# Performance work log

Measured on AMD Instinct MI355X. Metric: run time of the kernel, lower is better.

The kernel has to match this reference:

```python
import jax, jax.numpy as jnp
import numpy as np

G = 2   # FlipGroup order
H = 16  # num_heads
TEMPERATURE = 1.0


def _shared_w(A, B):
    # Z2 regular-representation equivariant linear: block-circulant weight
    # W = [[A, B], [B, A]], shape (dim, dim)
    return jnp.concatenate([
        jnp.concatenate([A, B], axis=1),
        jnp.concatenate([B, A], axis=1),
    ], axis=0)


def setup_inputs() -> dict:
    key = jax.random.key(0)
    ks = jax.random.split(key, 9)
    d = 1024
    dh = d // G
    inp = {"x": jax.random.normal(ks[0], (4, 1024, d), jnp.float32)}
    for i, n in enumerate(["wqA", "wqB", "wkA", "wkB", "wvA", "wvB", "wpA", "wpB"]):
        inp[n] = jax.random.normal(ks[i + 1], (dh, dh), jnp.float32) * 0.02
    return inp


def reference(x, wqA, wqB, wkA, wkB, wvA, wvB, wpA, wpB):
    B, N, C = x.shape
    hd = C // G // H            # per-group-channel head dim
    scale = hd ** -0.5

    q = x @ _shared_w(wqA, wqB).T
    k = x @ _shared_w(wkA, wkB).T
    v = x @ _shared_w(wvA, wvB).T

    def split(t):
        # (B,N,C) -> (B,H,G,N,hd): per-head features split into G group channels
        return t.reshape(B, N, H, G, hd).transpose(0, 2, 3, 1, 4)

    q, k, v = split(q), split(k), split(v)

    # per-channel attention: independent softmax per (head, group-channel)
    attn = jax.nn.softmax(
        jnp.einsum('bhgnd,bhgmd->bhgnm', q, k) * (scale / TEMPERATURE), axis=-1)
    o = jnp.einsum('bhgnm,bhgmd->bhgnd', attn, v)

    o = o.transpose(0, 3, 1, 2, 4).reshape(B, N, C)
    return o @ _shared_w(wpA, wpB).T
```

## Files before the change

kernel.cpp:

```cpp
#include <hip/hip_runtime.h>


typedef unsigned short ushort_t;
typedef __attribute__((ext_vector_type(4))) unsigned short ushort4_t;
typedef __attribute__((ext_vector_type(8))) unsigned short ushort8;
typedef __attribute__((ext_vector_type(8))) __bf16 bf16x8;
typedef __attribute__((ext_vector_type(4))) float f32x4;
typedef __attribute__((ext_vector_type(4))) unsigned int uint4_t;

#define GPTR(p) ((const __attribute__((address_space(1))) void*)(p))
#define LPTR(p) ((__attribute__((address_space(3))) void*)(p))

static __device__ __forceinline__ unsigned short f2b(float f) {
  unsigned int u = __builtin_bit_cast(unsigned int, f);
  unsigned int r = u + 0x7fffu + ((u >> 16) & 1u);
  return (unsigned short)(r >> 16);
}
static __device__ __forceinline__ float b2f(ushort_t h) {
  unsigned int u = ((unsigned int)h) << 16;
  return __builtin_bit_cast(float, u);
}
static __device__ __forceinline__ unsigned int pack2_rtna(float a, float b) {
  const unsigned int ra = __builtin_bit_cast(unsigned int, a) + 0x8000u;
  const unsigned int rb = __builtin_bit_cast(unsigned int, b) + 0x8000u;
  return __builtin_amdgcn_perm(rb, ra, 0x07060302u);
}

__global__ __launch_bounds__(256) void prep_k(
    const float* __restrict__ x,
    const float* __restrict__ wqA, const float* __restrict__ wqB,
    const float* __restrict__ wkA, const float* __restrict__ wkB,
    const float* __restrict__ wvA, const float* __restrict__ wvB,
    const float* __restrict__ wpA, const float* __restrict__ wpB,
    ushort_t* __restrict__ xsd, ushort_t* __restrict__ Wsd, float sclq) {
  const int bid = blockIdx.x;
  if (bid < 1024) {
    const int u = bid * 256 + threadIdx.x;
    const int m = u >> 6;
    const int k8 = (u & 63) * 8;
    const float* p1 = x + (size_t)m * 1024 + k8;
    const float* p2 = p1 + 512;
    const f32x4 a0 = *(const f32x4*)p1,  a1 = *(const f32x4*)(p1 + 4);
    const f32x4 b0 = *(const f32x4*)p2,  b1 = *(const f32x4*)(p2 + 4);
    ushort8 vs, vd;
#pragma unroll
    for (int e = 0; e < 4; ++e) {
      vs[e] = f2b(a0[e] + b0[e]); vs[e + 4] = f2b(a1[e] + b1[e]);
      vd[e] = f2b(a0[e] - b0[e]); vd[e + 4] = f2b(a1[e] - b1[e]);
    }
    *(ushort8*)&xsd[(size_t)m * 1024 + k8] = vs;
    *(ushort8*)&xsd[(size_t)m * 1024 + 512 + k8] = vd;
  } else {
    const int u = (bid - 1024) * 256 + threadIdx.x;
    const int hm = u >> 15;
    const int rem = u & 32767;
    const int r = rem >> 6;
    const int c8 = (rem & 63) * 8;
    const int proj = hm >> 1, isD = hm & 1;
    const float* A; const float* B;
    if (proj == 0)      { A = wqA; B = wqB; }
    else if (proj == 1) { A = wkA; B = wkB; }
    else if (proj == 2) { A = wvA; B = wvB; }
    else                { A = wpA; B = wpB; }
    const float scl = 0.5f * (proj == 0 ? sclq : 1.0f);
    const f32x4 a0 = *(const f32x4*)(A + (size_t)r * 512 + c8);
    const f32x4 a1 = *(const f32x4*)(A + (size_t)r * 512 + c8 + 4);
    const f32x4 b0 = *(const f32x4*)(B + (size_t)r * 512 + c8);
    const f32x4 b1 = *(const f32x4*)(B + (size_t)r * 512 + c8 + 4);
    ushort8 v;
#pragma unroll
    for (int e = 0; e < 4; ++e) {
      v[e]     = f2b(isD ? (a0[e] - b0[e]) * scl : (a0[e] + b0[e]) * scl);
      v[e + 4] = f2b(isD ? (a1[e] - b1[e]) * scl : (a1[e] + b1[e]) * scl);
    }
    *(ushort8*)&Wsd[(size_t)(proj * 1024 + isD * 512 + r) * 512 + c8] = v;
  }
}

__global__ __launch_bounds__(256, 3) void gemm_sd_qkv(const ushort_t* __restrict__ xsd,
                                                      const ushort_t* __restrict__ Wsd,
                                                      ushort_t* __restrict__ Qb,
                                                      ushort_t* __restrict__ Kb,
                                                      ushort_t* __restrict__ Vtb) {
  __shared__ ushort_t sh[24576];

  const int t = threadIdx.x;
  const int wid = t >> 6, lane = t & 63;
  const int wm = wid >> 1, half = wid & 1;
  const int lr = lane & 15, lg = lane >> 4;

  const int bid = blockIdx.x;
  const int c = bid & 7, j = bid >> 3;
  const int mt = c * 4 + (j & 3);
  const int nzt = j >> 2;
  const int z = nzt >> 3;
  const int n0 = (nzt & 7) * 64;
  const int m0 = mt * 128;

  f32x4 acc[4][4];
  const f32x4 fz = {0.f, 0.f, 0.f, 0.f};
#pragma unroll
  for (int mf = 0; mf < 4; ++mf)
#pragma unroll
    for (int nf = 0; nf < 4; ++nf) acc[mf][nf] = fz;

#define ISSUE(kt_, s_)                                                                   \
  {                                                                                      \
    ushort_t* base_ = sh + (s_) * 12288;                                                 \
    const int k0_ = (kt_) * 32;                                                          \
    _Pragma("unroll") for (int rnd = 0; rnd < 2; ++rnd) {                                \
      const int ch = rnd * 256 + t;                                                      \
      const int row = ch >> 2, cs = ch & 3;                                              \
      const int gcol = k0_ + ((cs ^ ((row >> 1) & 3)) << 3);                             \
      __builtin_amdgcn_global_load_lds(GPTR(xsd + (size_t)(m0 + row) * 1024 + gcol),     \
                                       LPTR(base_ + (size_t)ch * 8), 16, 0, 0);          \
      __builtin_amdgcn_global_load_lds(GPTR(xsd + (size_t)(m0 + row) * 1024 + 512 + gcol),\
                                       LPTR(base_ + 4096 + (size_t)ch * 8), 16, 0, 0);   \
    }                                                                                    \
    {                                                                                    \
      const int row = t >> 2, cs = t & 3;                                                \
      const int gcol = k0_ + ((cs ^ ((row >> 1) & 3)) << 3);                             \
      __builtin_amdgcn_global_load_lds(                                                  \
          GPTR(Wsd + (size_t)(z * 1024 + n0 + row) * 512 + gcol),                        \
          LPTR(sh + (s_) * 12288 + 8192 + (size_t)t * 8), 16, 0, 0);                     \
      __builtin_amdgcn_global_load_lds(                                                  \
          GPTR(Wsd + (size_t)(z * 1024 + 512 + n0 + row) * 512 + gcol),                  \
          LPTR(sh + (s_) * 12288 + 10240 + (size_t)t * 8), 16, 0, 0);                    \
    }                                                                                    \
  }

  ISSUE(0, 0)
  for (int kt = 0; kt < 16; ++kt) {
    const int s = kt & 1;
    asm volatile("" ::: "memory");
    __builtin_amdgcn_s_barrier();
    asm volatile("" ::: "memory");
    if (kt < 15) {
      ISSUE(kt + 1, s ^ 1)
      asm volatile("s_waitcnt vmcnt(6)" ::: "memory");
    } else {
      asm volatile("s_waitcnt vmcnt(0)" ::: "memory");
    }
    __builtin_amdgcn_sched_barrier(0);
    __builtin_amdgcn_s_barrier();
    asm volatile("" ::: "memory");

    const ushort_t* base = sh + s * 12288;
    const ushort_t* Asl = base + half * 4096;
    const ushort_t* Bsl = base + 8192 + half * 2048;
    bf16x8 a[4], b[4];
#pragma unroll
    for (int mf = 0; mf < 4; ++mf) {
      const int row = wm * 64 + mf * 16 + lr;
      a[mf] = *(const bf16x8*)&Asl[row * 32 + ((lg ^ ((row >> 1) & 3)) << 3)];
    }
#pragma unroll
    for (int nf = 0; nf < 4; ++nf) {
      const int row = nf * 16 + lr;
      b[nf] = *(const bf16x8*)&Bsl[row * 32 + ((lg ^ ((row >> 1) & 3)) << 3)];
    }
    __builtin_amdgcn_s_setprio(1);
#pragma unroll
    for (int mf = 0; mf < 4; ++mf)
#pragma unroll
      for (int nf = 0; nf < 4; ++nf)
        acc[mf][nf] = __builtin_amdgcn_mfma_f32_16x16x32_bf16(a[mf], b[nf], acc[mf][nf], 0, 0, 0);
    __builtin_amdgcn_s_setprio(0);
  }
#undef ISSUE

  __syncthreads();
  const int PAD = (z < 2) ? 72 : 73;
  ushort_t* tus = sh;
  ushort_t* tvd = sh + 128 * PAD;
  {
    ushort_t* dst = half ? tvd : tus;
#pragma unroll
    for (int mf = 0; mf < 4; ++mf)
#pragma unroll
      for (int nf = 0; nf < 4; ++nf)
#pragma unroll
        for (int rr = 0; rr < 4; ++rr) {
          const int row = wm * 64 + mf * 16 + lg * 4 + rr;
          const int col = nf * 16 + lr;
          dst[row * PAD + col] = f2b(acc[mf][nf][rr]);
        }
  }
  __syncthreads();

  if (z < 2) {
    ushort_t* C = (z == 0) ? Qb : Kb;
#pragma unroll
    for (int it = 0; it < 4; ++it) {
      const int idx = it * 256 + t;
      const int row = idx >> 3;
      const int c8 = (idx & 7) * 8;
      const ushort8 u8 = *(const ushort8*)&tus[row * 72 + c8];
      const ushort8 v8 = *(const ushort8*)&tvd[row * 72 + c8];
      ushort8 y1, y2;
#pragma unroll
      for (int e = 0; e < 8; ++e) {
        const float us = b2f(u8[e]), vd = b2f(v8[e]);
        y1[e] = f2b(us + vd);
        y2[e] = f2b(us - vd);
      }
      *(ushort8*)&C[(size_t)(m0 + row) * 1024 + n0 + c8] = y1;
      *(ushort8*)&C[(size_t)(m0 + row) * 1024 + 512 + n0 + c8] = y2;
    }
  } else {
    const int bidx = m0 >> 10, tok0 = m0 & 1023;
#pragma unroll
    for (int it = 0; it < 4; ++it) {
      const int idx = it * 256 + t;
      const int cr = idx >> 4;
      const int mc = (idx & 15) * 8;
      float y1v[8], y2v[8];
#pragma unroll
      for (int e = 0; e < 8; ++e) {
        const float us = b2f(tus[(mc + e) * 73 + cr]);
        const float vd = b2f(tvd[(mc + e) * 73 + cr]);
        y1v[e] = us + vd;
        y2v[e] = us - vd;
      }
      const int k6 = mc & 63;
      const int base = (k6 & 0x20) | ((k6 & 8) << 1) | ((k6 & 0x10) >> 2);
      const size_t rb1 = (size_t)bidx * 1024 * 1024 + (size_t)(n0 + cr) * 1024 +
                         tok0 + (mc & ~63) + base;
      const size_t rb2 = (size_t)bidx * 1024 * 1024 + (size_t)(512 + n0 + cr) * 1024 +
                         tok0 + (mc & ~63) + base;
      ushort4_t lo1, hi1, lo2, hi2;
#pragma unroll
      for (int e = 0; e < 4; ++e) {
        lo1[e] = f2b(y1v[e]); hi1[e] = f2b(y1v[e + 4]);
        lo2[e] = f2b(y2v[e]); hi2[e] = f2b(y2v[e + 4]);
      }
      *(ushort4_t*)&Vtb[rb1] = lo1;  *(ushort4_t*)&Vtb[rb1 + 8] = hi1;
      *(ushort4_t*)&Vtb[rb2] = lo2;  *(ushort4_t*)&Vtb[rb2 + 8] = hi2;
    }
  }
}

__global__ __launch_bounds__(512, 4) void attn_k(const ushort_t* __restrict__ Q,
                                                 const ushort_t* __restrict__ K,
                                                 const ushort_t* __restrict__ Vt,
                                                 ushort_t* __restrict__ Osd) {
  __shared__ ushort_t shmem[32768];
  ushort_t* KsL = shmem;
  ushort_t* VsL = shmem + 16384;
  float* obuf = (float*)shmem;

  const int t = threadIdx.x;
  const int w = t >> 6, lane = t & 63;
  const int hw = w >> 2;
  const int lr = lane & 15, lg = lane >> 4, lk8 = lg * 8;
  const int rkey = (lr >> 1) & 3;
  const int pkey = lr & 7;

  const int nlin = blockIdx.x;
  const int c = nlin & 7, j = nlin >> 3;
  const int p = c * 8 + (j >> 3);
  const int qb = j & 7;
  const int hp = p & 15, b = p >> 4;

  const size_t bbase = (size_t)b * 1024 * 1024;
  const size_t headc = (size_t)hp * 32 + hw * 512;
  const int q0 = qb * 128 + (w & 3) * 32;
  const f32x4 fzero = {0.f, 0.f, 0.f, 0.f};

  bf16x8 bq[2];
#pragma unroll
  for (int i = 0; i < 2; ++i)
    bq[i] = *(const bf16x8*)&Q[bbase + (size_t)(q0 + i * 16 + lr) * 1024 + headc + lk8];

  f32x4 oacc[2][2];
  float tq[2] = {0.f, 0.f};
#pragma unroll
  for (int i = 0; i < 2; ++i)
#pragma unroll
    for (int jj = 0; jj < 2; ++jj) oacc[i][jj] = fzero;

#define ISSUE_KV(kt_, s_)                                                                \
  {                                                                                      \
    ushort_t* Kd_ = KsL + (s_) * 4096;                                                   \
    ushort_t* Vd_ = VsL + (s_) * 4096;                                                   \
    const int hl = t >> 8, rem = t & 255;                                                \
    const size_t hc_ = (size_t)hp * 32 + hl * 512;                                       \
    const int krow = rem >> 2, kc = rem & 3;                                             \
    __builtin_amdgcn_global_load_lds(                                                    \
        GPTR(K + bbase + (size_t)((kt_) * 64 + krow) * 1024 + hc_ +                      \
             ((kc ^ ((krow >> 1) & 3)) << 3)),                                           \
        LPTR(Kd_ + (size_t)t * 8), 16, 0, 0);                                            \
    const int vrow = rem >> 3, vc = rem & 7;                                             \
    __builtin_amdgcn_global_load_lds(                                                    \
        GPTR(Vt + bbase + (size_t)(hc_ + vrow) * 1024 + (kt_) * 64 +                     \
             ((vc ^ (vrow & 7)) << 3)),                                                  \
        LPTR(Vd_ + (size_t)t * 8), 16, 0, 0);                                            \
  }

  ISSUE_KV(0, 0) ISSUE_KV(1, 1) ISSUE_KV(2, 2)
  for (int kt = 0; kt < 16; ++kt) {
    const int s = kt & 3;
    asm volatile("" ::: "memory");
    __builtin_amdgcn_s_barrier();
    asm volatile("" ::: "memory");
    if (kt < 13) {
      ISSUE_KV(kt + 3, (kt + 3) & 3)
      asm volatile("s_waitcnt vmcnt(6)" ::: "memory");
    } else if (kt == 13) {
      asm volatile("s_waitcnt vmcnt(4)" ::: "memory");
    } else if (kt == 14) {
      asm volatile("s_waitcnt vmcnt(2)" ::: "memory");
    } else {
      asm volatile("s_waitcnt vmcnt(0)" ::: "memory");
    }
    __builtin_amdgcn_sched_barrier(0);
    __builtin_amdgcn_s_barrier();
    asm volatile("" ::: "memory");

    const ushort_t* Ksb = KsL + s * 4096 + hw * 2048;
    const ushort_t* Vsb = VsL + s * 4096 + hw * 2048;

    bf16x8 ak[4];
#pragma unroll
    for (int kf = 0; kf < 4; ++kf)
      ak[kf] = *(const bf16x8*)&Ksb[(kf * 16 + lr) * 32 + ((lg ^ rkey) << 3)];

    bf16x8 ap[2][2];
#pragma unroll
    for (int i = 0; i < 2; ++i) {
      f32x4 s4[4];
      __builtin_amdgcn_s_setprio(1);
#pragma unroll
      for (int kf = 0; kf < 4; ++kf)
        s4[kf] = __builtin_amdgcn_mfma_f32_16x16x32_bf16(ak[kf], bq[i], fzero, 0, 0, 0);
      __builtin_amdgcn_s_setprio(0);
#pragma unroll
      for (int ks = 0; ks < 2; ++ks) {
        const float p0 = __builtin_amdgcn_exp2f(s4[2 * ks][0]);
        const float p1 = __builtin_amdgcn_exp2f(s4[2 * ks][1]);
        const float p2 = __builtin_amdgcn_exp2f(s4[2 * ks][2]);
        const float p3 = __builtin_amdgcn_exp2f(s4[2 * ks][3]);
        const float p4 = __builtin_amdgcn_exp2f(s4[2 * ks + 1][0]);
        const float p5 = __builtin_amdgcn_exp2f(s4[2 * ks + 1][1]);
        const float p6 = __builtin_amdgcn_exp2f(s4[2 * ks + 1][2]);
        const float p7 = __builtin_amdgcn_exp2f(s4[2 * ks + 1][3]);
        tq[i] += ((p0 + p1) + (p2 + p3)) + ((p4 + p5) + (p6 + p7));
        uint4_t u;
        u[0] = pack2_rtna(p0, p1);
        u[1] = pack2_rtna(p2, p3);
        u[2] = pack2_rtna(p4, p5);
        u[3] = pack2_rtna(p6, p7);
        ap[i][ks] = __builtin_bit_cast(bf16x8, u);
      }
    }

#pragma unroll
    for (int ks = 0; ks < 2; ++ks) {
      bf16x8 bv0 = *(const bf16x8*)&Vsb[(0 * 16 + lr) * 64 + ((ks * 32 + lk8) ^ (pkey << 3))];
      bf16x8 bv1 = *(const bf16x8*)&Vsb[(1 * 16 + lr) * 64 + ((ks * 32 + lk8) ^ (pkey << 3))];
      __builtin_amdgcn_s_setprio(1);
#pragma unroll
      for (int i = 0; i < 2; ++i) {
        oacc[i][0] = __builtin_amdgcn_mfma_f32_16x16x32_bf16(ap[i][ks], bv0, oacc[i][0], 0, 0, 0);
        oacc[i][1] = __builtin_amdgcn_mfma_f32_16x16x32_bf16(ap[i][ks], bv1, oacc[i][1], 0, 0, 0);
      }
      __builtin_amdgcn_s_setprio(0);
    }
  }
#undef ISSUE_KV

#pragma unroll
  for (int i = 0; i < 2; ++i) {
    tq[i] += __shfl_xor(tq[i], 16, 64);
    tq[i] += __shfl_xor(tq[i], 32, 64);
  }

  __syncthreads();
#pragma unroll
  for (int i = 0; i < 2; ++i) {
    float inv[4];
#pragma unroll
    for (int r = 0; r < 4; ++r)
      inv[r] = 1.0f / __shfl(tq[i], lg * 4 + r, 64);
#pragma unroll
    for (int jj = 0; jj < 2; ++jj)
#pragma unroll
      for (int r = 0; r < 4; ++r) {
        const int row = (w & 3) * 32 + i * 16 + lg * 4 + r;
        obuf[hw * 4224 + row * 33 + jj * 16 + lr] = oacc[i][jj][r] * inv[r];
      }
  }
  __syncthreads();

  {
    const int row = t >> 2;
    const int c8 = (t & 3) * 8;
    ushort8 vs, vd;
#pragma unroll
    for (int e = 0; e < 8; ++e) {
      const float o0 = obuf[0 * 4224 + row * 33 + c8 + e];
      const float o1 = obuf[1 * 4224 + row * 33 + c8 + e];
      vs[e] = f2b(o0 + o1);
      vd[e] = f2b(o0 - o1);
    }
    const size_t rowg = bbase + (size_t)(qb * 128 + row) * 1024;
    *(ushort8*)&Osd[rowg + hp * 32 + c8] = vs;
    *(ushort8*)&Osd[rowg + 512 + hp * 32 + c8] = vd;
  }
}

__global__ __launch_bounds__(256, 4) void gemm_out_sd(const ushort_t* __restrict__ Osd,
                                                      const ushort_t* __restrict__ Wsd,
                                                      float* __restrict__ out) {
  __shared__ ushort_t sh[24576];

  const int t = threadIdx.x;
  const int w = t >> 6, lane = t & 63;
  const int wm = w >> 1, half = w & 1;
  const int lr = lane & 15, lg = lane >> 4;

  const int bid = blockIdx.x;
  const int c = bid & 7, j = bid >> 3;
  const int mt = c * 8 + (j & 7);
  const int st = j >> 3;
  const int m0 = mt * 64, n0s = st * 64;

  f32x4 acc[2][4];
  const f32x4 fz = {0.f, 0.f, 0.f, 0.f};
#pragma unroll
  for (int mf = 0; mf < 2; ++mf)
#pragma unroll
    for (int nf = 0; nf < 4; ++nf) acc[mf][nf] = fz;

#define ISSUE_O(kt_, s_)                                                                 \
  {                                                                                      \
    ushort_t* base_ = sh + (s_) * 8192;                                                  \
    const int k0_ = (kt_) * 32;                                                          \
    const int row = t >> 2, kc = t & 3;                                                  \
    const int gcol = k0_ + ((kc ^ ((row >> 1) & 3)) << 3);                               \
    __builtin_amdgcn_global_load_lds(GPTR(Osd + (size_t)(m0 + row) * 1024 + gcol),       \
                                     LPTR(base_ + (size_t)t * 8), 16, 0, 0);             \
    __builtin_amdgcn_global_load_lds(GPTR(Osd + (size_t)(m0 + row) * 1024 + 512 + gcol), \
                                     LPTR(base_ + 2048 + (size_t)t * 8), 16, 0, 0);      \
    __builtin_amdgcn_global_load_lds(                                                    \
        GPTR(Wsd + (size_t)(3072 + n0s + row) * 512 + gcol),                             \
        LPTR(base_ + 4096 + (size_t)t * 8), 16, 0, 0);                                   \
    __builtin_amdgcn_global_load_lds(                                                    \
        GPTR(Wsd + (size_t)(3072 + 512 + n0s + row) * 512 + gcol),                       \
        LPTR(base_ + 6144 + (size_t)t * 8), 16, 0, 0);                                   \
  }

  ISSUE_O(0, 0) ISSUE_O(1, 1)
  int s = 0;
  for (int kt = 0; kt < 16; ++kt) {
    asm volatile("" ::: "memory");
    __builtin_amdgcn_s_barrier();
    asm volatile("" ::: "memory");
    if (kt < 14) {
      const int s2 = (s >= 1) ? s - 1 : 2;
      ISSUE_O(kt + 2, s2)
      asm volatile("s_waitcnt vmcnt(8)" ::: "memory");
    } else if (kt == 14) {
      asm volatile("s_waitcnt vmcnt(4)" ::: "memory");
    } else {
      asm volatile("s_waitcnt vmcnt(0)" ::: "memory");
    }
    __builtin_amdgcn_sched_barrier(0);
    __builtin_amdgcn_s_barrier();
    asm volatile("" ::: "memory");

    const ushort_t* base = sh + s * 8192;
    const ushort_t* Asl = base + half * 2048;
    const ushort_t* Bsl = base + 4096 + half * 2048;
    bf16x8 a[2], b[4];
#pragma unroll
    for (int mf = 0; mf < 2; ++mf) {
      const int row = wm * 32 + mf * 16 + lr;
      a[mf] = *(const bf16x8*)&Asl[row * 32 + ((lg ^ ((row >> 1) & 3)) << 3)];
    }
#pragma unroll
    for (int nf = 0; nf < 4; ++nf) {
      const int row = nf * 16 + lr;
      b[nf] = *(const bf16x8*)&Bsl[row * 32 + ((lg ^ ((row >> 1) & 3)) << 3)];
    }
    __builtin_amdgcn_s_setprio(1);
#pragma unroll
    for (int mf = 0; mf < 2; ++mf)
#pragma unroll
      for (int nf = 0; nf < 4; ++nf)
        acc[mf][nf] = __builtin_amdgcn_mfma_f32_16x16x32_bf16(a[mf], b[nf], acc[mf][nf], 0, 0, 0);
    __builtin_amdgcn_s_setprio(0);
    s = (s == 2) ? 0 : s + 1;
  }
#undef ISSUE_O

  __syncthreads();
  float* vdbuf = (float*)sh;
  if (half == 1) {
#pragma unroll
    for (int mf = 0; mf < 2; ++mf)
#pragma unroll
      for (int nf = 0; nf < 4; ++nf)
#pragma unroll
        for (int rr = 0; rr < 4; ++rr) {
          const int row = wm * 32 + mf * 16 + lg * 4 + rr;
          const int col = nf * 16 + lr;
          vdbuf[row * 66 + col] = acc[mf][nf][rr];
        }
  }
  __syncthreads();
  if (half == 0) {
#pragma unroll
    for (int mf = 0; mf < 2; ++mf)
#pragma unroll
      for (int nf = 0; nf < 4; ++nf)
#pragma unroll
        for (int rr = 0; rr < 4; ++rr) {
          const int row = wm * 32 + mf * 16 + lg * 4 + rr;
          const int col = nf * 16 + lr;
          const float us = acc[mf][nf][rr];
          const float vd = vdbuf[row * 66 + col];
          out[(size_t)(m0 + row) * 1024 + n0s + col] = us + vd;
          out[(size_t)(m0 + row) * 1024 + 512 + n0s + col] = us - vd;
        }
  }
}

extern "C" void kernel_launch(void* const* d_in, const int* in_sizes, int n_in,
                              void* d_out, int out_size, void* d_ws, size_t ws_size,
                              hipStream_t stream) {
  const float* x   = (const float*)d_in[0];
  const float* wqA = (const float*)d_in[1];
  const float* wqB = (const float*)d_in[2];
  const float* wkA = (const float*)d_in[3];
  const float* wkB = (const float*)d_in[4];
  const float* wvA = (const float*)d_in[5];
  const float* wvB = (const float*)d_in[6];
  const float* wpA = (const float*)d_in[7];
  const float* wpB = (const float*)d_in[8];
  float* out = (float*)d_out;

  const size_t NE = (size_t)4096 * 1024;
  ushort_t* Qb   = (ushort_t*)d_ws;
  ushort_t* Kb   = Qb + NE;
  ushort_t* Vtb  = Kb + NE;
  ushort_t* xsd  = Vtb + NE;
  ushort_t* Wsd  = xsd + NE;
  ushort_t* Osd  = xsd;

  const float SCL = 0.17677669529663687f * 1.4426950408889634f;

  prep_k<<<2048, 256, 0, stream>>>(x, wqA, wqB, wkA, wkB, wvA, wvB, wpA, wpB,
                                   xsd, Wsd, SCL);
  gemm_sd_qkv<<<768, 256, 0, stream>>>(xsd, Wsd, Qb, Kb, Vtb);
  attn_k<<<512, 512, 0, stream>>>(Qb, Kb, Vtb, Osd);
  gemm_out_sd<<<512, 256, 0, stream>>>(Osd, Wsd, out);

  (void)in_sizes; (void)n_in; (void)out_size; (void)ws_size;
}
```

Baseline: 79.11 us.

## Replace multi-stage LDS pipelines with single-buffer BK=64 loop in both projection GEMMs

Both the QKV projection GEMM and the output projection GEMM drop their double- and triple-buffered global-to-LDS prefetch pipelines. Each K iteration now loads a 64-wide K tile into a single LDS buffer, waits for all loads, computes two 32-wide MFMA sub-steps, then barriers. The XOR swizzle changes to an 8-chunk row pattern to match the wider tile. This halves the number of iterations and barriers, and cuts LDS use in the output GEMM, which could allow more resident blocks. In exchange, global load latency is no longer overlapped with MFMA work inside a block, so the kernels rely on occupancy across blocks to hide it.

```diff
diff --git a/kernel.cpp b/kernel.cpp
--- a/kernel.cpp
+++ b/kernel.cpp
@@ -104,72 +104,68 @@
 #pragma unroll
     for (int nf = 0; nf < 4; ++nf) acc[mf][nf] = fz;
 
-#define ISSUE(kt_, s_)                                                                   \
+#define ISSUE(kt_)                                                                       \
   {                                                                                      \
-    ushort_t* base_ = sh + (s_) * 12288;                                                 \
-    const int k0_ = (kt_) * 32;                                                          \
+    _Pragma("unroll") for (int rnd = 0; rnd < 4; ++rnd) {                                \
+      const int ch = rnd * 256 + t;                                                      \
+      const int row = ch >> 3, cs = ch & 7;                                              \
+      const int gcol = (kt_) * 64 + ((cs ^ (row & 7)) << 3);                             \
+      __builtin_amdgcn_global_load_lds(GPTR(xsd + (size_t)(m0 + row) * 1024 + gcol),     \
+                                       LPTR(sh + (size_t)ch * 8), 16, 0, 0);             \
+      __builtin_amdgcn_global_load_lds(GPTR(xsd + (size_t)(m0 + row) * 1024 + 512 + gcol),\
+                                       LPTR(sh + 8192 + (size_t)ch * 8), 16, 0, 0);      \
+    }                                                                                    \
     _Pragma("unroll") for (int rnd = 0; rnd < 2; ++rnd) {                                \
       const int ch = rnd * 256 + t;                                                      \
-      const int row = ch >> 2, cs = ch & 3;                                              \
-      const int gcol = k0_ + ((cs ^ ((row >> 1) & 3)) << 3);                             \
-      __builtin_amdgcn_global_load_lds(GPTR(xsd + (size_t)(m0 + row) * 1024 + gcol),     \
-                                       LPTR(base_ + (size_t)ch * 8), 16, 0, 0);          \
-      __builtin_amdgcn_global_load_lds(GPTR(xsd + (size_t)(m0 + row) * 1024 + 512 + gcol),\
-                                       LPTR(base_ + 4096 + (size_t)ch * 8), 16, 0, 0);   \
-    }                                                                                    \
-    {                                                                                    \
-      const int row = t >> 2, cs = t & 3;                                                \
-      const int gcol = k0_ + ((cs ^ ((row >> 1) & 3)) << 3);                             \
+      const int row = ch >> 3, cs = ch & 7;                                              \
+      const int gcol = (kt_) * 64 + ((cs ^ (row & 7)) << 3);                             \
       __builtin_amdgcn_global_load_lds(                                                  \
           GPTR(Wsd + (size_t)(z * 1024 + n0 + row) * 512 + gcol),                        \
-          LPTR(sh + (s_) * 12288 + 8192 + (size_t)t * 8), 16, 0, 0);                     \
+          LPTR(sh + 16384 + (size_t)ch * 8), 16, 0, 0);                                  \
       __builtin_amdgcn_global_load_lds(                                                  \
           GPTR(Wsd + (size_t)(z * 1024 + 512 + n0 + row) * 512 + gcol),                  \
-          LPTR(sh + (s_) * 12288 + 10240 + (size_t)t * 8), 16, 0, 0);                    \
+          LPTR(sh + 20480 + (size_t)ch * 8), 16, 0, 0);                                  \
     }                                                                                    \
   }
 
-  ISSUE(0, 0)
-  for (int kt = 0; kt < 16; ++kt) {
-    const int s = kt & 1;
-    asm volatile("" ::: "memory");
-    __builtin_amdgcn_s_barrier();
-    asm volatile("" ::: "memory");
-    if (kt < 15) {
-      ISSUE(kt + 1, s ^ 1)
-      asm volatile("s_waitcnt vmcnt(6)" ::: "memory");
-    } else {
-      asm volatile("s_waitcnt vmcnt(0)" ::: "memory");
-    }
+  const ushort_t* Asl = sh + half * 8192;
+  const ushort_t* Bsl = sh + 16384 + half * 4096;
+
+  for (int kt = 0; kt < 8; ++kt) {
+    ISSUE(kt)
+    asm volatile("s_waitcnt vmcnt(0)" ::: "memory");
     __builtin_amdgcn_sched_barrier(0);
     __builtin_amdgcn_s_barrier();
     asm volatile("" ::: "memory");
 
-    const ushort_t* base = sh + s * 12288;
-    const ushort_t* Asl = base + half * 4096;
-    const ushort_t* Bsl = base + 8192 + half * 2048;
-    bf16x8 a[4], b[4];
-#pragma unroll
-    for (int mf = 0; mf < 4; ++mf) {
-      const int row = wm * 64 + mf * 16 + lr;
-      a[mf] = *(const bf16x8*)&Asl[row * 32 + ((lg ^ ((row >> 1) & 3)) << 3)];
-    }
-#pragma unroll
-    for (int nf = 0; nf < 4; ++nf) {
-      const int row = nf * 16 + lr;
-      b[nf] = *(const bf16x8*)&Bsl[row * 32 + ((lg ^ ((row >> 1) & 3)) << 3)];
-    }
-    __builtin_amdgcn_s_setprio(1);
-#pragma unroll
-    for (int mf = 0; mf < 4; ++mf)
-#pragma unroll
-      for (int nf = 0; nf < 4; ++nf)
-        acc[mf][nf] = __builtin_amdgcn_mfma_f32_16x16x32_bf16(a[mf], b[nf], acc[mf][nf], 0, 0, 0);
-    __builtin_amdgcn_s_setprio(0);
+#pragma unroll
+    for (int kk = 0; kk < 2; ++kk) {
+      bf16x8 a[4], b[4];
+#pragma unroll
+      for (int mf = 0; mf < 4; ++mf) {
+        const int row = wm * 64 + mf * 16 + lr;
+        a[mf] = *(const bf16x8*)&Asl[row * 64 + (((kk * 4 + lg) ^ (row & 7)) << 3)];
+      }
+#pragma unroll
+      for (int nf = 0; nf < 4; ++nf) {
+        const int row = nf * 16 + lr;
+        b[nf] = *(const bf16x8*)&Bsl[row * 64 + (((kk * 4 + lg) ^ (row & 7)) << 3)];
+      }
+      __builtin_amdgcn_s_setprio(1);
+#pragma unroll
+      for (int mf = 0; mf < 4; ++mf)
+#pragma unroll
+        for (int nf = 0; nf < 4; ++nf)
+          acc[mf][nf] = __builtin_amdgcn_mfma_f32_16x16x32_bf16(a[mf], b[nf], acc[mf][nf], 0, 0, 0);
+      __builtin_amdgcn_s_setprio(0);
+    }
+    asm volatile("s_waitcnt lgkmcnt(0)" ::: "memory");
+    __builtin_amdgcn_sched_barrier(0);
+    __builtin_amdgcn_s_barrier();
+    asm volatile("" ::: "memory");
   }
 #undef ISSUE
 
-  __syncthreads();
   const int PAD = (z < 2) ? 72 : 73;
   ushort_t* tus = sh;
   ushort_t* tvd = sh + 128 * PAD;
@@ -412,7 +408,7 @@
 __global__ __launch_bounds__(256, 4) void gemm_out_sd(const ushort_t* __restrict__ Osd,
                                                       const ushort_t* __restrict__ Wsd,
                                                       float* __restrict__ out) {
-  __shared__ ushort_t sh[24576];
+  __shared__ ushort_t sh[16896];
 
   const int t = threadIdx.x;
   const int w = t >> 6, lane = t & 63;
@@ -432,69 +428,63 @@
 #pragma unroll
     for (int nf = 0; nf < 4; ++nf) acc[mf][nf] = fz;
 
-#define ISSUE_O(kt_, s_)                                                                 \
+#define ISSUE_O(kt_)                                                                     \
   {                                                                                      \
-    ushort_t* base_ = sh + (s_) * 8192;                                                  \
-    const int k0_ = (kt_) * 32;                                                          \
-    const int row = t >> 2, kc = t & 3;                                                  \
-    const int gcol = k0_ + ((kc ^ ((row >> 1) & 3)) << 3);                               \
-    __builtin_amdgcn_global_load_lds(GPTR(Osd + (size_t)(m0 + row) * 1024 + gcol),       \
-                                     LPTR(base_ + (size_t)t * 8), 16, 0, 0);             \
-    __builtin_amdgcn_global_load_lds(GPTR(Osd + (size_t)(m0 + row) * 1024 + 512 + gcol), \
-                                     LPTR(base_ + 2048 + (size_t)t * 8), 16, 0, 0);      \
-    __builtin_amdgcn_global_load_lds(                                                    \
-        GPTR(Wsd + (size_t)(3072 + n0s + row) * 512 + gcol),                             \
-        LPTR(base_ + 4096 + (size_t)t * 8), 16, 0, 0);                                   \
-    __builtin_amdgcn_global_load_lds(                                                    \
-        GPTR(Wsd + (size_t)(3072 + 512 + n0s + row) * 512 + gcol),                       \
-        LPTR(base_ + 6144 + (size_t)t * 8), 16, 0, 0);                                   \
-  }
-
-  ISSUE_O(0, 0) ISSUE_O(1, 1)
-  int s = 0;
-  for (int kt = 0; kt < 16; ++kt) {
-    asm volatile("" ::: "memory");
-    __builtin_amdgcn_s_barrier();
-    asm volatile("" ::: "memory");
-    if (kt < 14) {
-      const int s2 = (s >= 1) ? s - 1 : 2;
-      ISSUE_O(kt + 2, s2)
-      asm volatile("s_waitcnt vmcnt(8)" ::: "memory");
-    } else if (kt == 14) {
-      asm volatile("s_waitcnt vmcnt(4)" ::: "memory");
-    } else {
-      asm volatile("s_waitcnt vmcnt(0)" ::: "memory");
-    }
+    _Pragma("unroll") for (int rnd = 0; rnd < 2; ++rnd) {                                \
+      const int ch = rnd * 256 + t;                                                      \
+      const int row = ch >> 3, cs = ch & 7;                                              \
+      const int gcol = (kt_) * 64 + ((cs ^ (row & 7)) << 3);                             \
+      __builtin_amdgcn_global_load_lds(GPTR(Osd + (size_t)(m0 + row) * 1024 + gcol),     \
+                                       LPTR(sh + (size_t)ch * 8), 16, 0, 0);             \
+      __builtin_amdgcn_global_load_lds(GPTR(Osd + (size_t)(m0 + row) * 1024 + 512 + gcol),\
+                                       LPTR(sh + 4096 + (size_t)ch * 8), 16, 0, 0);      \
+      __builtin_amdgcn_global_load_lds(                                                  \
+          GPTR(Wsd + (size_t)(3072 + n0s + row) * 512 + gcol),                           \
+          LPTR(sh + 8192 + (size_t)ch * 8), 16, 0, 0);                                   \
+      __builtin_amdgcn_global_load_lds(                                                  \
+          GPTR(Wsd + (size_t)(3072 + 512 + n0s + row) * 512 + gcol),                     \
+          LPTR(sh + 12288 + (size_t)ch * 8), 16, 0, 0);                                  \
+    }                                                                                    \
+  }
+
+  const ushort_t* Asl = sh + half * 4096;
+  const ushort_t* Bsl = sh + 8192 + half * 4096;
+
+  for (int kt = 0; kt < 8; ++kt) {
+    ISSUE_O(kt)
+    asm volatile("s_waitcnt vmcnt(0)" ::: "memory");
     __builtin_amdgcn_sched_barrier(0);
     __builtin_amdgcn_s_barrier();
     asm volatile("" ::: "memory");
 
-    const ushort_t* base = sh + s * 8192;
-    const ushort_t* Asl = base + half * 2048;
-    const ushort_t* Bsl = base + 4096 + half * 2048;
-    bf16x8 a[2], b[4];
-#pragma unroll
-    for (int mf = 0; mf < 2; ++mf) {
-      const int row = wm * 32 + mf * 16 + lr;
-      a[mf] = *(const bf16x8*)&Asl[row * 32 + ((lg ^ ((row >> 1) & 3)) << 3)];
-    }
-#pragma unroll
-    for (int nf = 0; nf < 4; ++nf) {
-      const int row = nf * 16 + lr;
-      b[nf] = *(const bf16x8*)&Bsl[row * 32 + ((lg ^ ((row >> 1) & 3)) << 3)];
-    }
-    __builtin_amdgcn_s_setprio(1);
-#pragma unroll
-    for (int mf = 0; mf < 2; ++mf)
-#pragma unroll
-      for (int nf = 0; nf < 4; ++nf)
-        acc[mf][nf] = __builtin_amdgcn_mfma_f32_16x16x32_bf16(a[mf], b[nf], acc[mf][nf], 0, 0, 0);
-    __builtin_amdgcn_s_setprio(0);
-    s = (s == 2) ? 0 : s + 1;
+#pragma unroll
+    for (int kk = 0; kk < 2; ++kk) {
+      bf16x8 a[2], b[4];
+#pragma unroll
+      for (int mf = 0; mf < 2; ++mf) {
+        const int row = wm * 32 + mf * 16 + lr;
+        a[mf] = *(const bf16x8*)&Asl[row * 64 + (((kk * 4 + lg) ^ (row & 7)) << 3)];
+      }
+#pragma unroll
+      for (int nf = 0; nf < 4; ++nf) {
+        const int row = nf * 16 + lr;
+        b[nf] = *(const bf16x8*)&Bsl[row * 64 + (((kk * 4 + lg) ^ (row & 7)) << 3)];
+      }
+      __builtin_amdgcn_s_setprio(1);
+#pragma unroll
+      for (int mf = 0; mf < 2; ++mf)
+#pragma unroll
+        for (int nf = 0; nf < 4; ++nf)
+          acc[mf][nf] = __builtin_amdgcn_mfma_f32_16x16x32_bf16(a[mf], b[nf], acc[mf][nf], 0, 0, 0);
+      __builtin_amdgcn_s_setprio(0);
+    }
+    asm volatile("s_waitcnt lgkmcnt(0)" ::: "memory");
+    __builtin_amdgcn_sched_barrier(0);
+    __builtin_amdgcn_s_barrier();
+    asm volatile("" ::: "memory");
   }
 #undef ISSUE_O
 
-  __syncthreads();
   float* vdbuf = (float*)sh;
   if (half == 1) {
 #pragma unroll
```

New measurement: 77.38 us. -2.2%, faster.
